# Kernel tuning notes

Hardware: AMD Instinct MI355X
Metric: run time of the kernel (lower is better)

Reference implementation:

```python
import jax, jax.numpy as jnp
import numpy as np

D_MODEL = 1024
H = 16
D_K = D_MODEL // H
NEG = -1e9


def setup_inputs() -> dict:
    key = jax.random.key(0)
    ks = jax.random.split(key, 13)
    B, S = 4, 2048
    q = jax.random.normal(ks[0], (B, S, D_MODEL), dtype=jnp.float32)
    k = jax.random.normal(ks[1], (B, S, D_MODEL), dtype=jnp.float32)
    v = jax.random.normal(ks[2], (B, S, D_MODEL), dtype=jnp.float32)
    mask = jax.random.randint(ks[3], (B, 1, S, S), 0, 2, dtype=jnp.int32)
    s = 1.0 / np.sqrt(D_MODEL)
    wq = jax.random.uniform(ks[4], (D_MODEL, D_MODEL), jnp.float32, -s, s)
    bq = jax.random.uniform(ks[5], (D_MODEL,), jnp.float32, -s, s)
    wk = jax.random.uniform(ks[6], (D_MODEL, D_MODEL), jnp.float32, -s, s)
    bk = jax.random.uniform(ks[7], (D_MODEL,), jnp.float32, -s, s)
    wv = jax.random.uniform(ks[8], (D_MODEL, D_MODEL), jnp.float32, -s, s)
    bv = jax.random.uniform(ks[9], (D_MODEL,), jnp.float32, -s, s)
    wo = jax.random.uniform(ks[10], (D_MODEL, D_MODEL), jnp.float32, -s, s)
    bo = jax.random.uniform(ks[11], (D_MODEL,), jnp.float32, -s, s)
    return {"q": q, "k": k, "v": v, "mask": mask,
            "wq": wq, "bq": bq, "wk": wk, "bk": bk,
            "wv": wv, "bv": bv, "wo": wo, "bo": bo}


def reference(q, k, v, mask, wq, bq, wk, bk, wv, bv, wo, bo):
    B, S, _ = q.shape
    # projections (torch Linear: x @ W.T + b)
    query = q @ wq.T + bq
    key_ = k @ wk.T + bk
    value = v @ wv.T + bv
    # [B, S, H, D_K] -> [B, H, S, D_K]
    query = query.reshape(B, S, H, D_K).transpose(0, 2, 1, 3)
    key_ = key_.reshape(B, S, H, D_K).transpose(0, 2, 1, 3)
    value = value.reshape(B, S, H, D_K).transpose(0, 2, 1, 3)
    scores = jnp.einsum('bhqd,bhkd->bhqk', query, key_) / jnp.sqrt(jnp.float32(D_K))
    scores = jnp.where(mask == 0, jnp.float32(NEG), scores)
    attn = jax.nn.softmax(scores, axis=-1)  # dropout p=0 -> identity
    x = jnp.einsum('bhqk,bhkd->bhqd', attn, value)
    x = x.transpose(0, 2, 1, 3).reshape(B, S, D_MODEL)
    return x @ wo.T + bo
```

## Files before the change

kernel.cpp:

```cpp
#include <hip/hip_runtime.h>
#include <stdint.h>
#include <stddef.h>


typedef unsigned short ushort_t;
typedef unsigned long long u64;
typedef __attribute__((ext_vector_type(8))) short short8;
typedef __attribute__((ext_vector_type(4))) float floatx4;
typedef __attribute__((ext_vector_type(4))) unsigned short ushort4v;
typedef __attribute__((ext_vector_type(4))) unsigned int uint4v;

#define QSCALE (0.125f * 1.4426950408889634f)

__device__ __forceinline__ ushort_t f2bf(float f) {
    union { float ff; unsigned int i; } v; v.ff = f;
    unsigned int u = v.i;
    return (ushort_t)((u + 0x7fffu + ((u >> 16) & 1u)) >> 16);
}
__device__ __forceinline__ unsigned int pk2(float a, float b) {
    unsigned int r;
    asm("v_cvt_pk_bf16_f32 %0, %1, %2" : "=v"(r) : "v"(a), "v"(b));
    return r;
}
__device__ __forceinline__ float fexp2(float x) {
#if __has_builtin(__builtin_amdgcn_exp2f)
    return __builtin_amdgcn_exp2f(x);
#else
    return exp2f(x);
#endif
}
__device__ __forceinline__ void g2l16(const void* g, void* l) {
    __builtin_amdgcn_global_load_lds(
        (const __attribute__((address_space(1))) void*)(uintptr_t)g,
        (__attribute__((address_space(3))) void*)(uint32_t)(uintptr_t)l,
        16, 0, 0);
}

__global__ __launch_bounds__(256) void conv_w4(
    const float* __restrict__ w0, const float* __restrict__ w1,
    const float* __restrict__ w2, const float* __restrict__ w3,
    ushort_t* __restrict__ out)
{
    const int seg = blockIdx.y;
    const float* src = (seg == 0) ? w0 : (seg == 1) ? w1 : (seg == 2) ? w2 : w3;
    const int i = blockIdx.x * 256 + threadIdx.x;
    const float4 v = ((const float4*)src)[i];
    ushort4v o;
    o.x = f2bf(v.x); o.y = f2bf(v.y); o.z = f2bf(v.z); o.w = f2bf(v.w);
    ((ushort4v*)(out + (size_t)seg * 1024 * 1024))[i] = o;
}

__global__ __launch_bounds__(256) void cvt_a(
    const float* __restrict__ q, const float* __restrict__ k,
    const float* __restrict__ v,
    ushort_t* __restrict__ Qb, ushort_t* __restrict__ Kb,
    ushort_t* __restrict__ Vb)
{
    const int z = blockIdx.y;
    const float* src = (z == 0) ? q : (z == 1) ? k : v;
    ushort_t* dst = (z == 0) ? Qb : (z == 1) ? Kb : Vb;
    const int i = blockIdx.x * 256 + threadIdx.x;
    const float4 f0 = ((const float4*)src)[i * 2];
    const float4 f1 = ((const float4*)src)[i * 2 + 1];
    uint4v c;
    c.x = pk2(f0.x, f0.y); c.y = pk2(f0.z, f0.w);
    c.z = pk2(f1.x, f1.y); c.w = pk2(f1.z, f1.w);
    ((uint4v*)dst)[i] = c;
}

__global__ __launch_bounds__(256) void mask_pack(
    const int* __restrict__ m, u64* __restrict__ out)
{
    const int gid = blockIdx.x * 256 + threadIdx.x;
    const u64 bits = __ballot(m[gid] != 0);
    if ((threadIdx.x & 63) == 0) out[gid >> 6] = bits;
}

__device__ __forceinline__ void gemm_core(
    const ushort_t* __restrict__ Ain, const ushort_t* __restrict__ W,
    const float* __restrict__ bias, void* __restrict__ Cout,
    float scale, int mode)
{
    constexpr int N = 1024, K = 1024;
    __shared__ alignas(16) ushort_t As[3][128 * 32];
    __shared__ alignas(16) ushort_t Bs[3][128 * 32];

    const int tid  = threadIdx.x;
    const int lane = tid & 63;
    const int w    = tid >> 6;
    const int quad = lane >> 4;
    const int l16  = lane & 15;
    const int wm = w >> 1, wn = w & 1;
    const int bm = blockIdx.x * 128, bn = blockIdx.y * 128;

    const int ar0 = tid >> 2,         acs0 = ((tid & 3) ^ (ar0 & 3)) * 8;
    const int ar1 = (tid + 256) >> 2, acs1 = ((tid & 3) ^ (ar1 & 3)) * 8;
    const ushort_t* Ast0 = Ain + (size_t)(bm + ar0) * K + acs0;
    const ushort_t* Ast1 = Ain + (size_t)(bm + ar1) * K + acs1;
    const ushort_t* Wst0 = W + (size_t)(bn + ar0) * K + acs0;
    const ushort_t* Wst1 = W + (size_t)(bn + ar1) * K + acs1;

    const int ksw = (quad ^ (l16 & 3)) * 8;
    int asoff[4], bsoff[4];
#pragma unroll
    for (int i = 0; i < 4; i++) {
        asoff[i] = (wm * 64 + i * 16 + l16) * 32 + ksw;
        bsoff[i] = (wn * 64 + i * 16 + l16) * 32 + ksw;
    }

    floatx4 acc[4][4] = {};

    g2l16(Ast0,      &As[0][tid * 8]);
    g2l16(Ast1,      &As[0][(tid + 256) * 8]);
    g2l16(Wst0,      &Bs[0][tid * 8]);
    g2l16(Wst1,      &Bs[0][(tid + 256) * 8]);
    g2l16(Ast0 + 32, &As[1][tid * 8]);
    g2l16(Ast1 + 32, &As[1][(tid + 256) * 8]);
    g2l16(Wst0 + 32, &Bs[1][tid * 8]);
    g2l16(Wst1 + 32, &Bs[1][(tid + 256) * 8]);

#define GITER(SLOT, NSLOT, KOFF, DO_ISSUE, TOPW) do {                         \
    asm volatile("s_waitcnt " TOPW);                                          \
    asm volatile("s_waitcnt lgkmcnt(0)");                                     \
    __builtin_amdgcn_sched_barrier(0);                                        \
    __builtin_amdgcn_s_barrier();                                             \
    __builtin_amdgcn_sched_barrier(0);                                        \
    if (DO_ISSUE) {                                                           \
        g2l16(Ast0 + (KOFF), &As[NSLOT][tid * 8]);                            \
        g2l16(Ast1 + (KOFF), &As[NSLOT][(tid + 256) * 8]);                    \
        g2l16(Wst0 + (KOFF), &Bs[NSLOT][tid * 8]);                            \
        g2l16(Wst1 + (KOFF), &Bs[NSLOT][(tid + 256) * 8]);                    \
    }                                                                         \
    {                                                                         \
        short8 af[4], bf[4];                                                  \
        _Pragma("unroll")                                                     \
        for (int i = 0; i < 4; i++) af[i] = *(const short8*)&As[SLOT][asoff[i]];\
        _Pragma("unroll")                                                     \
        for (int i = 0; i < 4; i++) bf[i] = *(const short8*)&Bs[SLOT][bsoff[i]];\
        _Pragma("unroll")                                                     \
        for (int mi = 0; mi < 4; mi++)                                        \
        _Pragma("unroll")                                                     \
        for (int ni = 0; ni < 4; ni++)                                        \
            acc[mi][ni] = __builtin_amdgcn_mfma_f32_16x16x32_bf16(            \
                af[mi], bf[ni], acc[mi][ni], 0, 0, 0);                        \
    }                                                                         \
} while (0)

    for (int j = 0; j < 10; ++j) {
        const int kt = j * 96;
        GITER(0, 2, kt + 64,  true, "vmcnt(4)");
        GITER(1, 0, kt + 96,  true, "vmcnt(4)");
        GITER(2, 1, kt + 128, true, "vmcnt(4)");
    }
    GITER(0, 0, 0, false, "vmcnt(4)");
    GITER(1, 0, 0, false, "vmcnt(0)");
#undef GITER

#pragma unroll
    for (int ni = 0; ni < 4; ni++) {
        const int n = bn + wn * 64 + ni * 16 + l16;
        const float bv_ = bias[n];
#pragma unroll
        for (int mi = 0; mi < 4; mi++) {
            const int mbase = bm + wm * 64 + mi * 16 + quad * 4;
            if (mode == 2) {
                const int b_ = mbase >> 11, s0 = mbase & 2047;
                const int h = n >> 6, d = n & 63;
                ushort4v pk_;
#pragma unroll
                for (int r = 0; r < 4; r++)
                    pk_[r] = f2bf((acc[mi][ni][r] + bv_) * scale);
                *(ushort4v*)&((ushort_t*)Cout)[
                    (((size_t)(b_ * 16 + h)) * 64 + d) * 2048 + s0] = pk_;
            } else {
#pragma unroll
                for (int r = 0; r < 4; r++) {
                    const int m = mbase + r;
                    const float of = (acc[mi][ni][r] + bv_) * scale;
                    if (mode == 0) {
                        ((float*)Cout)[(size_t)m * N + n] = of;
                    } else {
                        const int b_ = m >> 11, s = m & 2047;
                        const int h = n >> 6, d = n & 63;
                        ((ushort_t*)Cout)[(((size_t)(b_ * 16 + h)) * 2048 + s) * 64 + d]
                            = f2bf(of);
                    }
                }
            }
        }
    }
}

__global__ __launch_bounds__(256, 3) void gemm_qkv(
    const ushort_t* __restrict__ Qb, const ushort_t* __restrict__ Kb,
    const ushort_t* __restrict__ Vb, const ushort_t* __restrict__ Wb,
    const float* __restrict__ bq, const float* __restrict__ bk,
    const float* __restrict__ bv,
    ushort_t* __restrict__ Qp, ushort_t* __restrict__ Kp,
    ushort_t* __restrict__ Vtp)
{
    const int z = blockIdx.z;
    const ushort_t* A = (z == 0) ? Qb : (z == 1) ? Kb : Vb;
    const ushort_t* W = Wb + (size_t)z * 1024 * 1024;
    const float* bi = (z == 0) ? bq : (z == 1) ? bk : bv;
    void* C = (z == 0) ? (void*)Qp : (z == 1) ? (void*)Kp : (void*)Vtp;
    const float sc = (z == 0) ? QSCALE : 1.0f;
    const int mode = (z == 2) ? 2 : 1;
    gemm_core(A, W, bi, C, sc, mode);
}

__global__ __launch_bounds__(256, 3) void gemm_out(
    const ushort_t* __restrict__ X, const ushort_t* __restrict__ W,
    const float* __restrict__ bo, float* __restrict__ out)
{
    gemm_core(X, W, bo, out, 1.0f, 0);
}

__global__ __launch_bounds__(256, 4) void attn(
    const ushort_t* __restrict__ Q,
    const ushort_t* __restrict__ Kk,
    const ushort_t* __restrict__ Vt,
    const u64* __restrict__ mb,
    ushort_t* __restrict__ X)
{
    constexpr int S = 2048;
    __shared__ alignas(16) ushort_t Ks[2][64 * 64];
    __shared__ alignas(16) ushort_t Vs[2][64 * 64];
    __shared__ alignas(16) ushort_t Ps[4][16 * 64];

    const int tid  = threadIdx.x;
    const int lane = tid & 63;
    const int w    = tid >> 6;
    const int quad = lane >> 4;
    const int l16  = lane & 15;
    const int bh = blockIdx.x;
    const int b  = bh >> 4, h = bh & 15;
    const int qbase = blockIdx.y * 64 + w * 16;
    const int qlane = qbase + l16;

    const int r0 = tid >> 3,         cs0 = ((tid & 7) ^ (r0 & 7)) * 8;
    const int r1 = (tid + 256) >> 3, cs1 = ((tid & 7) ^ (r1 & 7)) * 8;

    const ushort_t* Kst0 = &Kk[((size_t)bh * S + r0) * 64 + cs0];
    const ushort_t* Kst1 = &Kk[((size_t)bh * S + r1) * 64 + cs1];
    const ushort_t* Vst0 = &Vt[((size_t)bh * 64 + r0) * S + cs0];
    const ushort_t* Vst1 = &Vt[((size_t)bh * 64 + r1) * S + cs1];

    const int swz = l16 & 7;
    int kvoff[2][4], pfoff[2], pwoff[4];
#pragma unroll
    for (int ks = 0; ks < 2; ks++) {
        pfoff[ks] = l16 * 64 + (((ks * 4 + quad) ^ swz) * 8);
#pragma unroll
        for (int ni = 0; ni < 4; ni++)
            kvoff[ks][ni] = (ni * 16 + l16) * 64 + (((ks * 4 + quad) ^ swz) * 8);
    }
#pragma unroll
    for (int ni = 0; ni < 4; ni++)
        pwoff[ni] = l16 * 64 + (((ni * 2 + (quad >> 1)) ^ swz) * 8) + (quad & 1) * 4;
    ushort_t* Psw = &Ps[w][0];

    short8 qf[2];
#pragma unroll
    for (int ks = 0; ks < 2; ks++)
        qf[ks] = *(const short8*)&Q[((size_t)bh * S + qlane) * 64 + ks * 32 + quad * 8];

    short8 onesv;
#pragma unroll
    for (int i = 0; i < 8; i++) onesv[i] = (short)0x3F80;

    const u64* mrow = mb + ((size_t)b * S + qlane) * 32;

    floatx4 o[4] = {};
    floatx4 lf = {};

    g2l16(Kst0, &Ks[0][tid * 8]);
    g2l16(Kst1, &Ks[0][(tid + 256) * 8]);
    g2l16(Vst0, &Vs[0][tid * 8]);
    g2l16(Vst1, &Vs[0][(tid + 256) * 8]);
    __syncthreads();

    int cur = 0;
    for (int kt = 0; kt < 32; kt++) {
        if (kt < 31) {
            g2l16(Kst0 + (kt + 1) * 4096, &Ks[cur ^ 1][tid * 8]);
            g2l16(Kst1 + (kt + 1) * 4096, &Ks[cur ^ 1][(tid + 256) * 8]);
            g2l16(Vst0 + (kt + 1) * 64,   &Vs[cur ^ 1][tid * 8]);
            g2l16(Vst1 + (kt + 1) * 64,   &Vs[cur ^ 1][(tid + 256) * 8]);
        }
        const ushort_t* Ksc = &Ks[cur][0];
        const ushort_t* Vsc = &Vs[cur][0];

        floatx4 s[4] = {};
#pragma unroll
        for (int ks = 0; ks < 2; ks++)
#pragma unroll
            for (int ni = 0; ni < 4; ni++)
                s[ni] = __builtin_amdgcn_mfma_f32_16x16x32_bf16(
                    *(const short8*)&Ksc[kvoff[ks][ni]], qf[ks], s[ni], 0, 0, 0);

        const u64 mw = mrow[kt];
#pragma unroll
        for (int ni = 0; ni < 4; ni++) {
            const unsigned int t = (unsigned int)(mw >> (ni * 16 + quad * 4));
#pragma unroll
            for (int r = 0; r < 4; r++)
                s[ni][r] = (t & (1u << r)) ? fexp2(s[ni][r]) : 0.f;
        }

#pragma unroll
        for (int ni = 0; ni < 4; ni++) {
            const unsigned int lo = pk2(s[ni][0], s[ni][1]);
            const unsigned int hi = pk2(s[ni][2], s[ni][3]);
            const unsigned long long dv = ((unsigned long long)hi << 32) | lo;
            *(unsigned long long*)&Psw[pwoff[ni]] = dv;
        }

#pragma unroll
        for (int ks = 0; ks < 2; ks++) {
            const short8 pf = *(const short8*)&Psw[pfoff[ks]];
            lf = __builtin_amdgcn_mfma_f32_16x16x32_bf16(onesv, pf, lf, 0, 0, 0);
#pragma unroll
            for (int ni = 0; ni < 4; ni++)
                o[ni] = __builtin_amdgcn_mfma_f32_16x16x32_bf16(
                    *(const short8*)&Vsc[kvoff[ks][ni]], pf, o[ni], 0, 0, 0);
        }
        __syncthreads();
        cur ^= 1;
    }

    const float inv = 1.0f / lf[0];
#pragma unroll
    for (int ni = 0; ni < 4; ni++) {
        ushort4v pk_;
#pragma unroll
        for (int r = 0; r < 4; r++) pk_[r] = f2bf(o[ni][r] * inv);
        *(ushort4v*)&X[((size_t)b * S + qlane) * 1024 + h * 64 + ni * 16 + quad * 4] = pk_;
    }
}

extern "C" void kernel_launch(void* const* d_in, const int* in_sizes, int n_in,
                              void* d_out, int out_size, void* d_ws, size_t ws_size,
                              hipStream_t stream) {
    const float* q    = (const float*)d_in[0];
    const float* k    = (const float*)d_in[1];
    const float* v    = (const float*)d_in[2];
    const int*   mask = (const int*)d_in[3];
    const float* wq   = (const float*)d_in[4];
    const float* bq   = (const float*)d_in[5];
    const float* wk   = (const float*)d_in[6];
    const float* bk   = (const float*)d_in[7];
    const float* wv   = (const float*)d_in[8];
    const float* bv   = (const float*)d_in[9];
    const float* wo   = (const float*)d_in[10];
    const float* bo   = (const float*)d_in[11];

    const size_t MB = 1024 * 1024;
    uint8_t* ws = (uint8_t*)d_ws;
    ushort_t* Wb   = (ushort_t*)(ws);
    u64*      mbits= (u64*)(ws + 8 * MB);
    ushort_t* Qp   = (ushort_t*)(ws + 10 * MB);
    ushort_t* Kp   = (ushort_t*)(ws + 26 * MB);
    ushort_t* Vtp  = (ushort_t*)(ws + 42 * MB);
    ushort_t* Xp   = (ushort_t*)(ws + 58 * MB);
    ushort_t* Qb   = (ushort_t*)(ws + 58 * MB);
    ushort_t* Kb   = (ushort_t*)(ws + 74 * MB);
    ushort_t* Vb   = (ushort_t*)(ws + 90 * MB);

    dim3 blk(256);
    const int gW = (1024 * 1024) / 1024;
    const int gM = (4 * 2048 * 2048) / 256;

    conv_w4<<<dim3(gW, 4), blk, 0, stream>>>(wq, wk, wv, wo, Wb);
    mask_pack<<<gM, blk, 0, stream>>>(mask, mbits);
    cvt_a<<<dim3(4096, 3), blk, 0, stream>>>(q, k, v, Qb, Kb, Vb);

    gemm_qkv<<<dim3(64, 8, 3), blk, 0, stream>>>(Qb, Kb, Vb, Wb, bq, bk, bv,
                                                 Qp, Kp, Vtp);

    attn<<<dim3(64, 32), blk, 0, stream>>>(Qp, Kp, Vtp, mbits, Xp);

    gemm_out<<<dim3(64, 8), blk, 0, stream>>>(Xp, Wb + 3 * MB, bo, (float*)d_out);
}
```

Baseline: 419.5 us.

## Merge prep kernels, stagger A/W prefetch depth in GEMM, prioritize attention MFMAs

Three separate preprocessing launches (weight conversion, activation conversion, mask packing) are merged into one kernel, removing launch gaps and tail effects. The GEMM main loop now prefetches the activation tile three stages ahead and the weight tile one stage ahead, using four A buffers and two B buffers with a reworked wait-count schedule. The attention kernel raises wave priority around its MFMA blocks with s_setprio to favour matrix issue. The staggered prefetch changes LDS usage and depends on exact vmcnt accounting, which risks stalls or hazards if it is miscounted.

```diff
diff --git a/kernel.cpp b/kernel.cpp
--- a/kernel.cpp
+++ b/kernel.cpp
@@ -36,44 +36,46 @@
         16, 0, 0);
 }
 
-__global__ __launch_bounds__(256) void conv_w4(
-    const float* __restrict__ w0, const float* __restrict__ w1,
-    const float* __restrict__ w2, const float* __restrict__ w3,
-    ushort_t* __restrict__ out)
-{
-    const int seg = blockIdx.y;
-    const float* src = (seg == 0) ? w0 : (seg == 1) ? w1 : (seg == 2) ? w2 : w3;
-    const int i = blockIdx.x * 256 + threadIdx.x;
-    const float4 v = ((const float4*)src)[i];
-    ushort4v o;
-    o.x = f2bf(v.x); o.y = f2bf(v.y); o.z = f2bf(v.z); o.w = f2bf(v.w);
-    ((ushort4v*)(out + (size_t)seg * 1024 * 1024))[i] = o;
-}
-
-__global__ __launch_bounds__(256) void cvt_a(
+__global__ __launch_bounds__(256) void prep(
+    const float* __restrict__ wq, const float* __restrict__ wk,
+    const float* __restrict__ wv, const float* __restrict__ wo,
     const float* __restrict__ q, const float* __restrict__ k,
-    const float* __restrict__ v,
-    ushort_t* __restrict__ Qb, ushort_t* __restrict__ Kb,
-    ushort_t* __restrict__ Vb)
-{
-    const int z = blockIdx.y;
-    const float* src = (z == 0) ? q : (z == 1) ? k : v;
-    ushort_t* dst = (z == 0) ? Qb : (z == 1) ? Kb : Vb;
-    const int i = blockIdx.x * 256 + threadIdx.x;
-    const float4 f0 = ((const float4*)src)[i * 2];
-    const float4 f1 = ((const float4*)src)[i * 2 + 1];
-    uint4v c;
-    c.x = pk2(f0.x, f0.y); c.y = pk2(f0.z, f0.w);
-    c.z = pk2(f1.x, f1.y); c.w = pk2(f1.z, f1.w);
-    ((uint4v*)dst)[i] = c;
-}
-
-__global__ __launch_bounds__(256) void mask_pack(
-    const int* __restrict__ m, u64* __restrict__ out)
-{
-    const int gid = blockIdx.x * 256 + threadIdx.x;
-    const u64 bits = __ballot(m[gid] != 0);
-    if ((threadIdx.x & 63) == 0) out[gid >> 6] = bits;
+    const float* __restrict__ v, const int* __restrict__ mask,
+    ushort_t* __restrict__ Wb, ushort_t* __restrict__ Qb,
+    ushort_t* __restrict__ Kb, ushort_t* __restrict__ Vb,
+    u64* __restrict__ mbits)
+{
+    const int bx = blockIdx.x, tid = threadIdx.x;
+    if (bx < 14336) {
+        const float* src; ushort_t* dst; int idx;
+        if (bx < 2048) {
+            const int seg = bx >> 9;
+            src = (seg == 0) ? wq : (seg == 1) ? wk : (seg == 2) ? wv : wo;
+            dst = Wb + (size_t)seg * 1024 * 1024;
+            idx = (bx & 511) * 256 + tid;
+        } else {
+            const int b2 = bx - 2048;
+            const int z = b2 >> 12;
+            src = (z == 0) ? q : (z == 1) ? k : v;
+            dst = (z == 0) ? Qb : (z == 1) ? Kb : Vb;
+            idx = (b2 & 4095) * 256 + tid;
+        }
+        const float4 f0 = ((const float4*)src)[idx * 2];
+        const float4 f1 = ((const float4*)src)[idx * 2 + 1];
+        uint4v c;
+        c.x = pk2(f0.x, f0.y); c.y = pk2(f0.z, f0.w);
+        c.z = pk2(f1.x, f1.y); c.w = pk2(f1.z, f1.w);
+        ((uint4v*)dst)[idx] = c;
+    } else {
+        const int b3 = bx - 14336;
+        const int base = b3 * 4096;
+#pragma unroll
+        for (int it = 0; it < 16; ++it) {
+            const int gid = base + it * 256 + tid;
+            const u64 bits = __ballot(mask[gid] != 0);
+            if ((tid & 63) == 0) mbits[gid >> 6] = bits;
+        }
+    }
 }
 
 __device__ __forceinline__ void gemm_core(
@@ -82,8 +84,8 @@
     float scale, int mode)
 {
     constexpr int N = 1024, K = 1024;
-    __shared__ alignas(16) ushort_t As[3][128 * 32];
-    __shared__ alignas(16) ushort_t Bs[3][128 * 32];
+    __shared__ alignas(16) ushort_t As[4][128 * 32];
+    __shared__ alignas(16) ushort_t Bs[2][128 * 32];
 
     const int tid  = threadIdx.x;
     const int lane = tid & 63;
@@ -110,33 +112,38 @@
 
     floatx4 acc[4][4] = {};
 
+    g2l16(Wst0,      &Bs[0][tid * 8]);
+    g2l16(Wst1,      &Bs[0][(tid + 256) * 8]);
+    __builtin_amdgcn_sched_barrier(0);
     g2l16(Ast0,      &As[0][tid * 8]);
     g2l16(Ast1,      &As[0][(tid + 256) * 8]);
-    g2l16(Wst0,      &Bs[0][tid * 8]);
-    g2l16(Wst1,      &Bs[0][(tid + 256) * 8]);
     g2l16(Ast0 + 32, &As[1][tid * 8]);
     g2l16(Ast1 + 32, &As[1][(tid + 256) * 8]);
-    g2l16(Wst0 + 32, &Bs[1][tid * 8]);
-    g2l16(Wst1 + 32, &Bs[1][(tid + 256) * 8]);
-
-#define GITER(SLOT, NSLOT, KOFF, DO_ISSUE, TOPW) do {                         \
+    g2l16(Ast0 + 64, &As[2][tid * 8]);
+    g2l16(Ast1 + 64, &As[2][(tid + 256) * 8]);
+
+#define GITER(AS, WS, NW, NA, KW, KA, DO_W, DO_A, TOPW) do {                  \
     asm volatile("s_waitcnt " TOPW);                                          \
     asm volatile("s_waitcnt lgkmcnt(0)");                                     \
     __builtin_amdgcn_sched_barrier(0);                                        \
     __builtin_amdgcn_s_barrier();                                             \
     __builtin_amdgcn_sched_barrier(0);                                        \
-    if (DO_ISSUE) {                                                           \
-        g2l16(Ast0 + (KOFF), &As[NSLOT][tid * 8]);                            \
-        g2l16(Ast1 + (KOFF), &As[NSLOT][(tid + 256) * 8]);                    \
-        g2l16(Wst0 + (KOFF), &Bs[NSLOT][tid * 8]);                            \
-        g2l16(Wst1 + (KOFF), &Bs[NSLOT][(tid + 256) * 8]);                    \
+    if (DO_W) {                                                               \
+        g2l16(Wst0 + (KW), &Bs[NW][tid * 8]);                                 \
+        g2l16(Wst1 + (KW), &Bs[NW][(tid + 256) * 8]);                         \
     }                                                                         \
+    __builtin_amdgcn_sched_barrier(0);                                        \
+    if (DO_A) {                                                               \
+        g2l16(Ast0 + (KA), &As[NA][tid * 8]);                                 \
+        g2l16(Ast1 + (KA), &As[NA][(tid + 256) * 8]);                         \
+    }                                                                         \
+    __builtin_amdgcn_sched_barrier(0);                                        \
     {                                                                         \
         short8 af[4], bf[4];                                                  \
         _Pragma("unroll")                                                     \
-        for (int i = 0; i < 4; i++) af[i] = *(const short8*)&As[SLOT][asoff[i]];\
+        for (int i = 0; i < 4; i++) af[i] = *(const short8*)&As[AS][asoff[i]];\
         _Pragma("unroll")                                                     \
-        for (int i = 0; i < 4; i++) bf[i] = *(const short8*)&Bs[SLOT][bsoff[i]];\
+        for (int i = 0; i < 4; i++) bf[i] = *(const short8*)&Bs[WS][bsoff[i]];\
         _Pragma("unroll")                                                     \
         for (int mi = 0; mi < 4; mi++)                                        \
         _Pragma("unroll")                                                     \
@@ -146,14 +153,21 @@
     }                                                                         \
 } while (0)
 
-    for (int j = 0; j < 10; ++j) {
-        const int kt = j * 96;
-        GITER(0, 2, kt + 64,  true, "vmcnt(4)");
-        GITER(1, 0, kt + 96,  true, "vmcnt(4)");
-        GITER(2, 1, kt + 128, true, "vmcnt(4)");
-    }
-    GITER(0, 0, 0, false, "vmcnt(4)");
-    GITER(1, 0, 0, false, "vmcnt(0)");
+    GITER(0, 0, 1, 3,  32,  96, true, true, "vmcnt(4)");
+    GITER(1, 1, 0, 0,  64, 128, true, true, "vmcnt(2)");
+    GITER(2, 0, 1, 1,  96, 160, true, true, "vmcnt(2)");
+    GITER(3, 1, 0, 2, 128, 192, true, true, "vmcnt(2)");
+    for (int j = 1; j < 7; ++j) {
+        const int kb = j * 128;
+        GITER(0, 0, 1, 3, kb + 32,  kb + 96,  true, true, "vmcnt(2)");
+        GITER(1, 1, 0, 0, kb + 64,  kb + 128, true, true, "vmcnt(2)");
+        GITER(2, 0, 1, 1, kb + 96,  kb + 160, true, true, "vmcnt(2)");
+        GITER(3, 1, 0, 2, kb + 128, kb + 192, true, true, "vmcnt(2)");
+    }
+    GITER(0, 0, 1, 3, 928, 992, true,  true,  "vmcnt(2)");
+    GITER(1, 1, 0, 0, 960, 0,   true,  false, "vmcnt(2)");
+    GITER(2, 0, 1, 0, 992, 0,   true,  false, "vmcnt(0)");
+    GITER(3, 1, 0, 0, 0,   0,   false, false, "vmcnt(0)");
 #undef GITER
 
 #pragma unroll
@@ -292,12 +306,14 @@
         const ushort_t* Vsc = &Vs[cur][0];
 
         floatx4 s[4] = {};
+        __builtin_amdgcn_s_setprio(1);
 #pragma unroll
         for (int ks = 0; ks < 2; ks++)
 #pragma unroll
             for (int ni = 0; ni < 4; ni++)
                 s[ni] = __builtin_amdgcn_mfma_f32_16x16x32_bf16(
                     *(const short8*)&Ksc[kvoff[ks][ni]], qf[ks], s[ni], 0, 0, 0);
+        __builtin_amdgcn_s_setprio(0);
 
         const u64 mw = mrow[kt];
 #pragma unroll
@@ -316,6 +332,7 @@
             *(unsigned long long*)&Psw[pwoff[ni]] = dv;
         }
 
+        __builtin_amdgcn_s_setprio(1);
 #pragma unroll
         for (int ks = 0; ks < 2; ks++) {
             const short8 pf = *(const short8*)&Psw[pfoff[ks]];
@@ -325,6 +342,7 @@
                 o[ni] = __builtin_amdgcn_mfma_f32_16x16x32_bf16(
                     *(const short8*)&Vsc[kvoff[ks][ni]], pf, o[ni], 0, 0, 0);
         }
+        __builtin_amdgcn_s_setprio(0);
         __syncthreads();
         cur ^= 1;
     }
@@ -368,12 +386,9 @@
     ushort_t* Vb   = (ushort_t*)(ws + 90 * MB);
 
     dim3 blk(256);
-    const int gW = (1024 * 1024) / 1024;
-    const int gM = (4 * 2048 * 2048) / 256;
-
-    conv_w4<<<dim3(gW, 4), blk, 0, stream>>>(wq, wk, wv, wo, Wb);
-    mask_pack<<<gM, blk, 0, stream>>>(mask, mbits);
-    cvt_a<<<dim3(4096, 3), blk, 0, stream>>>(q, k, v, Qb, Kb, Vb);
+
+    prep<<<dim3(18432), blk, 0, stream>>>(wq, wk, wv, wo, q, k, v, mask,
+                                          Wb, Qb, Kb, Vb, mbits);
 
     gemm_qkv<<<dim3(64, 8, 3), blk, 0, stream>>>(Qb, Kb, Vb, Wb, bq, bk, bv,
                                                  Qp, Kp, Vtp);
```

Result: faster. 403.5 us, median of 2 (-3.8%).
